# Kernel optimization log

Hardware: AMD Instinct MI355X
Metric: run time of the kernel (lower is better)

Reference implementation:

```python
import jax, jax.numpy as jnp
from jax import lax
import numpy as np

B, N_MEL, T_MEL = 256, 80, 800
R = 16                      # n_frames_per_step
RNN = 1024                  # decoder_rnn_dim
ENC = 256                   # token_embedding_size
MEL_DIM = N_MEL * R         # 1280, == RNN + ENC (LSTMCell input size)
IN_DIM = RNN + ENC          # 1280


def setup_inputs() -> dict:
    key = jax.random.key(0)
    ks = jax.random.split(key, 10)
    s = 0.02
    return {
        "context": jax.random.normal(ks[0], (B, ENC), dtype=jnp.float32),
        "target": jax.random.normal(ks[1], (B, N_MEL, T_MEL), dtype=jnp.float32),
        "W_ih": jax.random.normal(ks[2], (4 * RNN, IN_DIM), dtype=jnp.float32) * s,
        "b_ih": jnp.zeros((4 * RNN,), dtype=jnp.float32),
        "W_hh": jax.random.normal(ks[3], (4 * RNN, RNN), dtype=jnp.float32) * s,
        "b_hh": jnp.zeros((4 * RNN,), dtype=jnp.float32),
        "W_proj": jax.random.normal(ks[4], (MEL_DIM, IN_DIM), dtype=jnp.float32) * s,
        "b_proj": jnp.zeros((MEL_DIM,), dtype=jnp.float32),
        "W_gate": jax.random.normal(ks[5], (1, IN_DIM), dtype=jnp.float32) * s,
        "b_gate": jnp.zeros((1,), dtype=jnp.float32),
    }


def _decoder_forward(context, target, W_ih, b_ih, W_hh, b_hh, W_proj, b_proj, W_gate, b_gate):
    b = context.shape[0]
    n_mel, t_mel = target.shape[1], target.shape[2]
    mel_dim = W_proj.shape[0]
    r = mel_dim // n_mel                      # n_frames_per_step
    T = t_mel // r                            # decoder steps
    rnn = W_hh.shape[1]

    # parse_decoder_inputs: [B, n_mel, T_mel] -> [T, B, mel_dim]
    frames = target.transpose(0, 2, 1).reshape(b, T, mel_dim).transpose(1, 0, 2)
    # step 0 uses the all-zeros go frame; step t>=1 uses target frame t (teacher forcing, p=1)
    inputs = frames.at[0].set(0.0)

    h0 = jnp.zeros((b, rnn), dtype=context.dtype)
    c0 = jnp.zeros((b, rnn), dtype=context.dtype)

    def step(carry, x):
        h, c = carry
        gates = x @ W_ih.T + b_ih + h @ W_hh.T + b_hh   # [B, 4*rnn]
        i, f, g, o = jnp.split(gates, 4, axis=-1)        # torch LSTMCell gate order
        c_new = jax.nn.sigmoid(f) * c + jax.nn.sigmoid(i) * jnp.tanh(g)
        h_new = jax.nn.sigmoid(o) * jnp.tanh(c_new)
        # eval mode: dropout on c is identity
        oc = jnp.concatenate([h_new, context], axis=1)   # [B, rnn+enc]
        mel = oc @ W_proj.T + b_proj                     # [B, mel_dim]
        gate = oc @ W_gate.T + b_gate                    # [B, 1]
        return (h_new, c_new), (mel, gate)

    _, (mels, gates) = lax.scan(step, (h0, c0), inputs)
    # mels: [T, B, mel_dim] -> [B, n_mel, T_mel]
    mel_outputs = mels.transpose(1, 0, 2).reshape(b, T * r, n_mel).transpose(0, 2, 1)
    gate_outputs = gates.transpose(1, 0, 2)              # [B, T, 1]
    return mel_outputs, gate_outputs


def reference(context, target, W_ih, b_ih, W_hh, b_hh, W_proj, b_proj, W_gate, b_gate):
    return _decoder_forward(context, target, W_ih, b_ih, W_hh, b_hh,
                            W_proj, b_proj, W_gate, b_gate)
```

## Files before the change

kernel.cpp:

```cpp
#include <hip/hip_runtime.h>
#include <hip/hip_bf16.h>
#include <math.h>

#define BB     256
#define NMEL   80
#define TMEL   800
#define NFR    16
#define TT     50
#define RNN    1024
#define ENC    256
#define INDIM  1280
#define G4     4096
#define MROWS  (TT*BB)

typedef __attribute__((ext_vector_type(8))) short bf16x8;
typedef __attribute__((ext_vector_type(4))) float f32x4;

#define GAS __attribute__((address_space(1)))
#define LAS __attribute__((address_space(3)))

__device__ __forceinline__ unsigned short f2bf(float f) {
    unsigned int u = __float_as_uint(f);
    u += 0x7FFFu + ((u >> 16) & 1u);
    return (unsigned short)(u >> 16);
}
__device__ __forceinline__ float bf2f(unsigned short s) {
    return __uint_as_float(((unsigned int)s) << 16);
}
__device__ __forceinline__ float fsig(float x) {
    return 1.f / (1.f + __expf(-x));
}
__device__ __forceinline__ float ftanh(float x) {
    return 2.f / (1.f + __expf(-2.f * x)) - 1.f;
}


__global__ void k_f32_to_bf16(const float* __restrict__ src,
                              unsigned short* __restrict__ dst, int n) {
    for (int i = blockIdx.x * blockDim.x + threadIdx.x; i < n;
         i += gridDim.x * blockDim.x)
        dst[i] = f2bf(src[i]);
}

__global__ void k_conv_wph(const float* __restrict__ wproj,
                           unsigned short* __restrict__ dst) {
    const int n = INDIM * RNN;
    for (int i = blockIdx.x * blockDim.x + threadIdx.x; i < n;
         i += gridDim.x * blockDim.x) {
        int mp = i >> 10, k = i & 1023;
        int mel = mp >> 4, fr = mp & 15;
        dst[i] = f2bf(wproj[(fr * NMEL + mel) * INDIM + k]);
    }
}

__global__ void k_frames(const float* __restrict__ target,
                         unsigned short* __restrict__ frames) {
    const int n = TT * BB * INDIM;
    for (int i = blockIdx.x * blockDim.x + threadIdx.x; i < n;
         i += gridDim.x * blockDim.x) {
        int k = i % INDIM;
        int rb = i / INDIM;
        int b = rb & (BB - 1);
        int t = rb >> 8;
        unsigned short v = 0;
        if (t > 0) {
            int mel = k % NMEL, fr = k / NMEL;
            v = f2bf(target[(b * NMEL + mel) * TMEL + t * NFR + fr]);
        }
        frames[i] = v;
    }
}

__global__ void k_ctxproj(const float* __restrict__ context,
                          const float* __restrict__ wproj,
                          const float* __restrict__ bproj,
                          float* __restrict__ ctx) {
    int i = blockIdx.x * blockDim.x + threadIdx.x;
    if (i >= BB * INDIM) return;
    int mp = i % INDIM, b = i / INDIM;
    int mel = mp >> 4, fr = mp & 15;
    int m = fr * NMEL + mel;
    const float* wr = wproj + (size_t)m * INDIM + RNN;
    const float* cb = context + b * ENC;
    float acc = bproj[m];
    for (int e = 0; e < ENC; ++e) acc += cb[e] * wr[e];
    ctx[(size_t)b * INDIM + mp] = acc;
}

__global__ void k_gatectx(const float* __restrict__ context,
                          const float* __restrict__ wgate,
                          const float* __restrict__ bgate,
                          float* __restrict__ gctx) {
    int b = blockIdx.x * blockDim.x + threadIdx.x;
    if (b >= BB) return;
    float acc = bgate[0];
    const float* cb = context + b * ENC;
    for (int e = 0; e < ENC; ++e) acc += cb[e] * wgate[RNN + e];
    gctx[b] = acc;
}

template<int STRIDE, int KDIM>
__device__ __forceinline__ void gemm_core(const unsigned short* __restrict__ A,
                                          const unsigned short* __restrict__ Bw,
                                          int mblk, int nblk,
                                          unsigned short* As, unsigned short* Bs,
                                          f32x4 acc[4][4]) {
    const int tid = threadIdx.x, lane = tid & 63, wid = tid >> 6;
    const int wm = (wid >> 1) * 64, wn = (wid & 1) * 64;
    const int lr = lane & 15, lko = (lane >> 4) * 8;
    const int c0 = wid * 128 + lane;
    const int c1 = c0 + 64;
    const int r0 = c0 >> 2, o0 = (c0 & 3) * 8;
    const int r1 = c1 >> 2, o1 = (c1 & 3) * 8;
    const unsigned short* a0p = A + (size_t)(mblk + r0) * STRIDE + o0;
    const unsigned short* a1p = A + (size_t)(mblk + r1) * STRIDE + o1;
    const unsigned short* b0p = Bw + (size_t)(nblk + r0) * STRIDE + o0;
    const unsigned short* b1p = Bw + (size_t)(nblk + r1) * STRIDE + o1;
    unsigned short* da0 = As + wid * 1024;
    unsigned short* da1 = As + wid * 1024 + 512;
    unsigned short* db0 = Bs + wid * 1024;
    unsigned short* db1 = Bs + wid * 1024 + 512;
    for (int k0 = 0; k0 < KDIM; k0 += 32) {
        __syncthreads();
        __builtin_amdgcn_global_load_lds((const GAS unsigned int*)(a0p + k0),
                                         (LAS unsigned int*)da0, 16, 0, 0);
        __builtin_amdgcn_global_load_lds((const GAS unsigned int*)(a1p + k0),
                                         (LAS unsigned int*)da1, 16, 0, 0);
        __builtin_amdgcn_global_load_lds((const GAS unsigned int*)(b0p + k0),
                                         (LAS unsigned int*)db0, 16, 0, 0);
        __builtin_amdgcn_global_load_lds((const GAS unsigned int*)(b1p + k0),
                                         (LAS unsigned int*)db1, 16, 0, 0);
        __syncthreads();
        bf16x8 af[4], bfv[4];
        #pragma unroll
        for (int mi = 0; mi < 4; ++mi)
            af[mi] = *(const bf16x8*)(As + (wm + mi * 16 + lr) * 32 + lko);
        #pragma unroll
        for (int ni = 0; ni < 4; ++ni)
            bfv[ni] = *(const bf16x8*)(Bs + (wn + ni * 16 + lr) * 32 + lko);
        #pragma unroll
        for (int mi = 0; mi < 4; ++mi)
            #pragma unroll
            for (int ni = 0; ni < 4; ++ni)
                acc[mi][ni] = __builtin_amdgcn_mfma_f32_16x16x32_bf16(
                    af[mi], bfv[ni], acc[mi][ni], 0, 0, 0);
    }
}

__global__ __launch_bounds__(256) void k_gemm_xproj(
    const unsigned short* __restrict__ A,
    const unsigned short* __restrict__ Bw,
    const float* __restrict__ b_ih, const float* __restrict__ b_hh,
    unsigned short* __restrict__ Cout)
{
    __shared__ unsigned short As[4096], Bs[4096];
    f32x4 acc[4][4] = {};
    const int mblk = blockIdx.y * 128, nblk = blockIdx.x * 128;
    gemm_core<INDIM, INDIM>(A, Bw, mblk, nblk, As, Bs, acc);
    const int lane = threadIdx.x & 63, wid = threadIdx.x >> 6;
    const int wm = (wid >> 1) * 64, wn = (wid & 1) * 64, lr = lane & 15;
    #pragma unroll
    for (int ni = 0; ni < 4; ++ni) {
        const int col = nblk + wn + ni * 16 + lr;
        const float bias = b_ih[col] + b_hh[col];
        #pragma unroll
        for (int mi = 0; mi < 4; ++mi) {
            const int row0 = mblk + wm + mi * 16 + (lane >> 4) * 4;
            #pragma unroll
            for (int r = 0; r < 4; ++r)
                Cout[(size_t)(row0 + r) * G4 + col] = f2bf(acc[mi][ni][r] + bias);
        }
    }
}

__global__ __launch_bounds__(256) void k_gemm_mel(
    const unsigned short* __restrict__ A,
    const unsigned short* __restrict__ Bw,
    const float* __restrict__ ctxproj,
    float* __restrict__ out0)
{
    __shared__ unsigned short As[4096], Bs[4096];
    __shared__ float txp[4][16][20];
    f32x4 acc[4][4] = {};
    const int mblk = blockIdx.y * 128, nblk = blockIdx.x * 128;
    gemm_core<RNN, RNN>(A, Bw, mblk, nblk, As, Bs, acc);
    const int lane = threadIdx.x & 63, wid = threadIdx.x >> 6;
    const int wm = (wid >> 1) * 64, wn = (wid & 1) * 64, lr = lane & 15;
    const int rbase = (lane >> 4) * 4;
    const int rowl = lane & 15, fq = lane >> 4;
    #pragma unroll
    for (int mi = 0; mi < 4; ++mi) {
        const int row0 = mblk + wm + mi * 16;
        const int t = row0 >> 8, b0 = row0 & 255;
        #pragma unroll
        for (int ni = 0; ni < 4; ++ni) {
            const int colbase = nblk + wn + ni * 16;
            const int mel = colbase >> 4;
            __syncthreads();
            #pragma unroll
            for (int r = 0; r < 4; ++r)
                txp[wid][rbase + r][lr] = acc[mi][ni][r];
            __syncthreads();
            const int bL = b0 + rowl;
            f32x4 v = *(const f32x4*)&txp[wid][rowl][fq * 4];
            f32x4 cx = *(const f32x4*)(ctxproj + (size_t)bL * INDIM +
                                       mel * 16 + fq * 4);
            *(f32x4*)(out0 + (size_t)(bL * NMEL + mel) * TMEL +
                      t * NFR + fq * 4) = v + cx;
        }
    }
}

__global__ __launch_bounds__(512) void k_step(
    const unsigned short* __restrict__ Whh,
    const unsigned short* __restrict__ xproj_t,
    const unsigned short* __restrict__ h_prev,
    unsigned short* __restrict__ h_next,
    float* __restrict__ c)
{
    __shared__ unsigned short Abuf[3][8192];
    __shared__ unsigned short Bbuf[3][8192];
    __shared__ unsigned short xg[4096];
    __shared__ float cld[64][16];
    __shared__ float gates[4][64][17];
    const int tid = threadIdx.x, lane = tid & 63, w = tid >> 6;
    const int g = w & 3, mh = w >> 2;
    const int n0 = blockIdx.x * 16, m0 = blockIdx.y * 64;
    const int lr = lane & 15, q = lane >> 4;

    const int cc1 = tid, cc2 = tid + 512;
    const int r1 = cc1 >> 4, s1g = (cc1 & 15) ^ (r1 & 15);
    const int r2 = cc2 >> 4, s2g = (cc2 & 15) ^ (r2 & 15);
    const unsigned short* a1src = h_prev + (size_t)(m0 + r1) * RNN + s1g * 8;
    const unsigned short* a2src = h_prev + (size_t)(m0 + r2) * RNN + s2g * 8;
    const unsigned short* b1src = Whh +
        (size_t)((r1 >> 4) * RNN + n0 + (r1 & 15)) * RNN + s1g * 8;
    const unsigned short* b2src = Whh +
        (size_t)((r2 >> 4) * RNN + n0 + (r2 & 15)) * RNN + s2g * 8;
    const unsigned short* xsrc = xproj_t +
        (size_t)(m0 + ((tid >> 1) & 63)) * G4 + (tid >> 7) * RNN + n0 +
        (tid & 1) * 8;
    const float* csrc = c + (size_t)(m0 + (tid >> 2)) * RNN + n0 + (tid & 3) * 4;

#define STAGE(buf, k0) do {                                                    \
    __builtin_amdgcn_global_load_lds((const GAS unsigned int*)(a1src + (k0)),  \
        (LAS unsigned int*)&Abuf[buf][w * 512], 16, 0, 0);                     \
    __builtin_amdgcn_global_load_lds((const GAS unsigned int*)(a2src + (k0)),  \
        (LAS unsigned int*)&Abuf[buf][4096 + w * 512], 16, 0, 0);              \
    __builtin_amdgcn_global_load_lds((const GAS unsigned int*)(b1src + (k0)),  \
        (LAS unsigned int*)&Bbuf[buf][w * 512], 16, 0, 0);                     \
    __builtin_amdgcn_global_load_lds((const GAS unsigned int*)(b2src + (k0)),  \
        (LAS unsigned int*)&Bbuf[buf][4096 + w * 512], 16, 0, 0); } while (0)

    if (w < 4)
        __builtin_amdgcn_global_load_lds((const GAS unsigned int*)csrc,
            (LAS unsigned int*)&cld[w * 16][0], 16, 0, 0);
    __builtin_amdgcn_global_load_lds((const GAS unsigned int*)xsrc,
        (LAS unsigned int*)&xg[w * 512], 16, 0, 0);
    STAGE(0, 0); STAGE(1, 128);

    f32x4 acc[2] = {};
    #pragma unroll
    for (int it = 0; it < 8; ++it) {
        if (it <= 5) STAGE((it + 2) % 3, (it + 2) * 128);
        if (it <= 5)      asm volatile("s_waitcnt vmcnt(8)" ::: "memory");
        else if (it == 6) asm volatile("s_waitcnt vmcnt(4)" ::: "memory");
        else              asm volatile("s_waitcnt vmcnt(0)" ::: "memory");
        asm volatile("s_barrier" ::: "memory");
        __builtin_amdgcn_sched_barrier(0);
        const unsigned short* Ab = Abuf[it % 3];
        const unsigned short* Bb = Bbuf[it % 3];
        #pragma unroll
        for (int ks = 0; ks < 4; ++ks) {
            const int j = ((ks * 4 + q) ^ lr) * 8;
            bf16x8 a0 = *(const bf16x8*)(Ab + (mh * 32 + lr) * 128 + j);
            bf16x8 a1 = *(const bf16x8*)(Ab + (mh * 32 + 16 + lr) * 128 + j);
            bf16x8 bv = *(const bf16x8*)(Bb + (g * 16 + lr) * 128 + j);
            acc[0] = __builtin_amdgcn_mfma_f32_16x16x32_bf16(a0, bv, acc[0], 0, 0, 0);
            acc[1] = __builtin_amdgcn_mfma_f32_16x16x32_bf16(a1, bv, acc[1], 0, 0, 0);
        }
        asm volatile("s_waitcnt lgkmcnt(0)" ::: "memory");
        __builtin_amdgcn_sched_barrier(0);
        asm volatile("s_barrier" ::: "memory");
    }

    #pragma unroll
    for (int mi = 0; mi < 2; ++mi)
        #pragma unroll
        for (int r = 0; r < 4; ++r) {
            const int row = mh * 32 + mi * 16 + q * 4 + r;
            gates[g][row][lr] = acc[mi][r] +
                bf2f(xg[(g * 64 + row) * 16 + lr]);
        }
    __syncthreads();

    #pragma unroll
    for (int q2 = 0; q2 < 2; ++q2) {
        const int e = tid + q2 * 512;
        const int row = e >> 4, col = e & 15;
        const int b = m0 + row, j = n0 + col;
        const float xi = gates[0][row][col];
        const float xf = gates[1][row][col];
        const float xgt = gates[2][row][col];
        const float xo = gates[3][row][col];
        const float si = fsig(xi);
        const float sf = fsig(xf);
        const float so = fsig(xo);
        const float cp = cld[row][col];
        const float cn = sf * cp + si * ftanh(xgt);
        const float hn = so * ftanh(cn);
        c[(size_t)b * RNN + j] = cn;
        h_next[(size_t)b * RNN + j] = f2bf(hn);
    }
#undef STAGE
}

__global__ void k_gate(const unsigned short* __restrict__ h,
                       const float* __restrict__ wgate,
                       const float* __restrict__ gctx,
                       float* __restrict__ out1) {
    const int gw = (blockIdx.x * blockDim.x + threadIdx.x) >> 6;
    const int lane = threadIdx.x & 63;
    if (gw >= MROWS) return;
    const unsigned short* hr = h + (size_t)gw * RNN + lane * 16;
    const float* wr = wgate + lane * 16;
    float acc = 0.f;
    #pragma unroll
    for (int j = 0; j < 16; ++j) acc += bf2f(hr[j]) * wr[j];
    for (int off = 32; off; off >>= 1) acc += __shfl_down(acc, off);
    if (lane == 0) {
        const int t = gw >> 8, b = gw & 255;
        out1[b * TT + t] = acc + gctx[b];
    }
}

static const size_t OFF_WIH   = 0;
static const size_t OFF_WHH   = OFF_WIH   + (size_t)G4 * INDIM * 2;
static const size_t OFF_WPH   = OFF_WHH   + (size_t)G4 * RNN * 2;
static const size_t OFF_FRM   = OFF_WPH   + (size_t)INDIM * RNN * 2;
static const size_t OFF_XPROJ = OFF_FRM   + (size_t)MROWS * INDIM * 2;
static const size_t OFF_HALL  = OFF_XPROJ + (size_t)MROWS * G4 * 2;
static const size_t OFF_C     = OFF_HALL  + (size_t)(TT + 1) * BB * RNN * 2;
static const size_t OFF_CTX   = OFF_C     + (size_t)BB * RNN * 4;
static const size_t OFF_GCTX  = OFF_CTX   + (size_t)BB * INDIM * 4;

extern "C" void kernel_launch(void* const* d_in, const int* in_sizes, int n_in,
                              void* d_out, int out_size, void* d_ws, size_t ws_size,
                              hipStream_t stream) {
    const float* context = (const float*)d_in[0];
    const float* target  = (const float*)d_in[1];
    const float* W_ih    = (const float*)d_in[2];
    const float* b_ih    = (const float*)d_in[3];
    const float* W_hh    = (const float*)d_in[4];
    const float* b_hh    = (const float*)d_in[5];
    const float* W_proj  = (const float*)d_in[6];
    const float* b_proj  = (const float*)d_in[7];
    const float* W_gate  = (const float*)d_in[8];
    const float* b_gate  = (const float*)d_in[9];
    float* out = (float*)d_out;
    char* ws = (char*)d_ws;

    unsigned short* wih_bf  = (unsigned short*)(ws + OFF_WIH);
    unsigned short* whh_bf  = (unsigned short*)(ws + OFF_WHH);
    unsigned short* wph_bf  = (unsigned short*)(ws + OFF_WPH);
    unsigned short* frames  = (unsigned short*)(ws + OFF_FRM);
    unsigned short* xproj   = (unsigned short*)(ws + OFF_XPROJ);
    unsigned short* h_all   = (unsigned short*)(ws + OFF_HALL);
    float*          c_buf   = (float*)(ws + OFF_C);
    float*          ctxproj = (float*)(ws + OFF_CTX);
    float*          gctx    = (float*)(ws + OFF_GCTX);

    hipMemsetAsync(h_all, 0, (size_t)BB * RNN * 2, stream);
    hipMemsetAsync(c_buf, 0, (size_t)BB * RNN * 4, stream);

    k_f32_to_bf16<<<2048, 256, 0, stream>>>(W_ih, wih_bf, G4 * INDIM);
    k_f32_to_bf16<<<2048, 256, 0, stream>>>(W_hh, whh_bf, G4 * RNN);
    k_conv_wph<<<2048, 256, 0, stream>>>(W_proj, wph_bf);
    k_frames<<<2048, 256, 0, stream>>>(target, frames);
    k_ctxproj<<<(BB * INDIM + 255) / 256, 256, 0, stream>>>(context, W_proj,
                                                            b_proj, ctxproj);
    k_gatectx<<<1, 256, 0, stream>>>(context, W_gate, b_gate, gctx);

    k_gemm_xproj<<<dim3(G4 / 128, MROWS / 128), 256, 0, stream>>>(
        frames, wih_bf, b_ih, b_hh, xproj);

    for (int t = 0; t < TT; ++t) {
        k_step<<<dim3(64, 4), 512, 0, stream>>>(
            whh_bf, xproj + (size_t)t * BB * G4,
            h_all + (size_t)t * BB * RNN,
            h_all + (size_t)(t + 1) * BB * RNN, c_buf);
    }

    k_gemm_mel<<<dim3(INDIM / 128, MROWS / 128), 256, 0, stream>>>(
        h_all + (size_t)BB * RNN, wph_bf, ctxproj, out);
    k_gate<<<MROWS / 4, 256, 0, stream>>>(h_all + (size_t)BB * RNN, W_gate,
                                          gctx, out + (size_t)BB * NMEL * TMEL);
}
```

Baseline: 856.9 us.

## Double-buffer and swizzle LDS in bulk GEMMs with 512-thread blocks and K=64 tiles

Replaces the single-buffered K=32 GEMM core used by the input-projection and mel-projection GEMMs with a double-buffered K=64 core. The next tile's global-to-LDS loads are issued before computing on the current one, and the LDS layout is XOR-swizzled to avoid bank conflicts. Blocks grow to 8 waves, each computing a 64x32 sub-tile, so each block has more waves to hide latency. LDS use per block roughly quadruples, and the hand-placed waitcnt and barrier sequencing is fragile.

```diff
diff --git a/kernel.cpp b/kernel.cpp
--- a/kernel.cpp
+++ b/kernel.cpp
@@ -100,72 +100,91 @@
 }
 
 template<int STRIDE, int KDIM>
-__device__ __forceinline__ void gemm_core(const unsigned short* __restrict__ A,
-                                          const unsigned short* __restrict__ Bw,
-                                          int mblk, int nblk,
-                                          unsigned short* As, unsigned short* Bs,
-                                          f32x4 acc[4][4]) {
-    const int tid = threadIdx.x, lane = tid & 63, wid = tid >> 6;
-    const int wm = (wid >> 1) * 64, wn = (wid & 1) * 64;
-    const int lr = lane & 15, lko = (lane >> 4) * 8;
-    const int c0 = wid * 128 + lane;
-    const int c1 = c0 + 64;
-    const int r0 = c0 >> 2, o0 = (c0 & 3) * 8;
-    const int r1 = c1 >> 2, o1 = (c1 & 3) * 8;
-    const unsigned short* a0p = A + (size_t)(mblk + r0) * STRIDE + o0;
-    const unsigned short* a1p = A + (size_t)(mblk + r1) * STRIDE + o1;
-    const unsigned short* b0p = Bw + (size_t)(nblk + r0) * STRIDE + o0;
-    const unsigned short* b1p = Bw + (size_t)(nblk + r1) * STRIDE + o1;
-    unsigned short* da0 = As + wid * 1024;
-    unsigned short* da1 = As + wid * 1024 + 512;
-    unsigned short* db0 = Bs + wid * 1024;
-    unsigned short* db1 = Bs + wid * 1024 + 512;
-    for (int k0 = 0; k0 < KDIM; k0 += 32) {
-        __syncthreads();
-        __builtin_amdgcn_global_load_lds((const GAS unsigned int*)(a0p + k0),
-                                         (LAS unsigned int*)da0, 16, 0, 0);
-        __builtin_amdgcn_global_load_lds((const GAS unsigned int*)(a1p + k0),
-                                         (LAS unsigned int*)da1, 16, 0, 0);
-        __builtin_amdgcn_global_load_lds((const GAS unsigned int*)(b0p + k0),
-                                         (LAS unsigned int*)db0, 16, 0, 0);
-        __builtin_amdgcn_global_load_lds((const GAS unsigned int*)(b1p + k0),
-                                         (LAS unsigned int*)db1, 16, 0, 0);
-        __syncthreads();
-        bf16x8 af[4], bfv[4];
+__device__ __forceinline__ void gemm_core2(const unsigned short* __restrict__ A,
+                                           const unsigned short* __restrict__ Bw,
+                                           int mblk, int nblk,
+                                           unsigned short* As,
+                                           unsigned short* Bs,
+                                           f32x4 acc[4][2]) {
+    const int tid = threadIdx.x, lane = tid & 63, w = tid >> 6;
+    const int lr = lane & 15, q = lane >> 4;
+    const int wm = (w >> 2) * 64, wn = (w & 3) * 32;
+    const int cc1 = tid, cc2 = tid + 512;
+    const int r1 = cc1 >> 3, s1 = ((cc1 & 7) ^ (r1 & 7)) * 8;
+    const int r2 = cc2 >> 3, s2 = ((cc2 & 7) ^ (r2 & 7)) * 8;
+    const unsigned short* a1p = A + (size_t)(mblk + r1) * STRIDE + s1;
+    const unsigned short* a2p = A + (size_t)(mblk + r2) * STRIDE + s2;
+    const unsigned short* b1p = Bw + (size_t)(nblk + r1) * STRIDE + s1;
+    const unsigned short* b2p = Bw + (size_t)(nblk + r2) * STRIDE + s2;
+
+#define GSTAGE(buf, k0) do {                                                   \
+    __builtin_amdgcn_global_load_lds((const GAS unsigned int*)(a1p + (k0)),    \
+        (LAS unsigned int*)(As + (buf) * 8192 + w * 512), 16, 0, 0);           \
+    __builtin_amdgcn_global_load_lds((const GAS unsigned int*)(a2p + (k0)),    \
+        (LAS unsigned int*)(As + (buf) * 8192 + 4096 + w * 512), 16, 0, 0);    \
+    __builtin_amdgcn_global_load_lds((const GAS unsigned int*)(b1p + (k0)),    \
+        (LAS unsigned int*)(Bs + (buf) * 8192 + w * 512), 16, 0, 0);           \
+    __builtin_amdgcn_global_load_lds((const GAS unsigned int*)(b2p + (k0)),    \
+        (LAS unsigned int*)(Bs + (buf) * 8192 + 4096 + w * 512), 16, 0, 0); } while (0)
+
+    constexpr int NIT = KDIM / 64;
+    GSTAGE(0, 0);
+    #pragma unroll 4
+    for (int it = 0; it < NIT; ++it) {
+        if (it < NIT - 1) {
+            GSTAGE((it + 1) & 1, (it + 1) * 64);
+            asm volatile("s_waitcnt vmcnt(4)" ::: "memory");
+        } else {
+            asm volatile("s_waitcnt vmcnt(0)" ::: "memory");
+        }
+        asm volatile("s_barrier" ::: "memory");
+        __builtin_amdgcn_sched_barrier(0);
+        const unsigned short* Ab = As + (it & 1) * 8192;
+        const unsigned short* Bb = Bs + (it & 1) * 8192;
         #pragma unroll
-        for (int mi = 0; mi < 4; ++mi)
-            af[mi] = *(const bf16x8*)(As + (wm + mi * 16 + lr) * 32 + lko);
-        #pragma unroll
-        for (int ni = 0; ni < 4; ++ni)
-            bfv[ni] = *(const bf16x8*)(Bs + (wn + ni * 16 + lr) * 32 + lko);
-        #pragma unroll
-        for (int mi = 0; mi < 4; ++mi)
+        for (int ks = 0; ks < 2; ++ks) {
+            const int j = (((ks * 4 + q) ^ (lr & 7)) * 8);
+            bf16x8 af[4], bv[2];
             #pragma unroll
-            for (int ni = 0; ni < 4; ++ni)
-                acc[mi][ni] = __builtin_amdgcn_mfma_f32_16x16x32_bf16(
-                    af[mi], bfv[ni], acc[mi][ni], 0, 0, 0);
-    }
-}
-
-__global__ __launch_bounds__(256) void k_gemm_xproj(
+            for (int mi = 0; mi < 4; ++mi)
+                af[mi] = *(const bf16x8*)(Ab + (wm + mi * 16 + lr) * 64 + j);
+            #pragma unroll
+            for (int ni = 0; ni < 2; ++ni)
+                bv[ni] = *(const bf16x8*)(Bb + (wn + ni * 16 + lr) * 64 + j);
+            #pragma unroll
+            for (int mi = 0; mi < 4; ++mi)
+                #pragma unroll
+                for (int ni = 0; ni < 2; ++ni)
+                    acc[mi][ni] = __builtin_amdgcn_mfma_f32_16x16x32_bf16(
+                        af[mi], bv[ni], acc[mi][ni], 0, 0, 0);
+        }
+        asm volatile("s_waitcnt lgkmcnt(0)" ::: "memory");
+        __builtin_amdgcn_sched_barrier(0);
+        asm volatile("s_barrier" ::: "memory");
+    }
+#undef GSTAGE
+}
+
+__global__ __launch_bounds__(512) void k_gemm_xproj(
     const unsigned short* __restrict__ A,
     const unsigned short* __restrict__ Bw,
     const float* __restrict__ b_ih, const float* __restrict__ b_hh,
     unsigned short* __restrict__ Cout)
 {
-    __shared__ unsigned short As[4096], Bs[4096];
-    f32x4 acc[4][4] = {};
+    __shared__ unsigned short As[2][8192], Bs[2][8192];
+    f32x4 acc[4][2] = {};
     const int mblk = blockIdx.y * 128, nblk = blockIdx.x * 128;
-    gemm_core<INDIM, INDIM>(A, Bw, mblk, nblk, As, Bs, acc);
-    const int lane = threadIdx.x & 63, wid = threadIdx.x >> 6;
-    const int wm = (wid >> 1) * 64, wn = (wid & 1) * 64, lr = lane & 15;
-    #pragma unroll
-    for (int ni = 0; ni < 4; ++ni) {
+    gemm_core2<INDIM, INDIM>(A, Bw, mblk, nblk, &As[0][0], &Bs[0][0], acc);
+    const int lane = threadIdx.x & 63, w = threadIdx.x >> 6;
+    const int wm = (w >> 2) * 64, wn = (w & 3) * 32;
+    const int lr = lane & 15, q = lane >> 4;
+    #pragma unroll
+    for (int ni = 0; ni < 2; ++ni) {
         const int col = nblk + wn + ni * 16 + lr;
         const float bias = b_ih[col] + b_hh[col];
         #pragma unroll
         for (int mi = 0; mi < 4; ++mi) {
-            const int row0 = mblk + wm + mi * 16 + (lane >> 4) * 4;
+            const int row0 = mblk + wm + mi * 16 + q * 4;
             #pragma unroll
             for (int r = 0; r < 4; ++r)
                 Cout[(size_t)(row0 + r) * G4 + col] = f2bf(acc[mi][ni][r] + bias);
@@ -173,36 +192,37 @@
     }
 }
 
-__global__ __launch_bounds__(256) void k_gemm_mel(
+__global__ __launch_bounds__(512) void k_gemm_mel(
     const unsigned short* __restrict__ A,
     const unsigned short* __restrict__ Bw,
     const float* __restrict__ ctxproj,
     float* __restrict__ out0)
 {
-    __shared__ unsigned short As[4096], Bs[4096];
-    __shared__ float txp[4][16][20];
-    f32x4 acc[4][4] = {};
+    __shared__ unsigned short As[2][8192], Bs[2][8192];
+    __shared__ float txp[8][16][20];
+    f32x4 acc[4][2] = {};
     const int mblk = blockIdx.y * 128, nblk = blockIdx.x * 128;
-    gemm_core<RNN, RNN>(A, Bw, mblk, nblk, As, Bs, acc);
-    const int lane = threadIdx.x & 63, wid = threadIdx.x >> 6;
-    const int wm = (wid >> 1) * 64, wn = (wid & 1) * 64, lr = lane & 15;
-    const int rbase = (lane >> 4) * 4;
+    gemm_core2<RNN, RNN>(A, Bw, mblk, nblk, &As[0][0], &Bs[0][0], acc);
+    const int lane = threadIdx.x & 63, w = threadIdx.x >> 6;
+    const int wm = (w >> 2) * 64, wn = (w & 3) * 32;
+    const int lr = lane & 15, q = lane >> 4;
+    const int rbase = q * 4;
     const int rowl = lane & 15, fq = lane >> 4;
     #pragma unroll
     for (int mi = 0; mi < 4; ++mi) {
         const int row0 = mblk + wm + mi * 16;
         const int t = row0 >> 8, b0 = row0 & 255;
         #pragma unroll
-        for (int ni = 0; ni < 4; ++ni) {
+        for (int ni = 0; ni < 2; ++ni) {
             const int colbase = nblk + wn + ni * 16;
             const int mel = colbase >> 4;
             __syncthreads();
             #pragma unroll
             for (int r = 0; r < 4; ++r)
-                txp[wid][rbase + r][lr] = acc[mi][ni][r];
+                txp[w][rbase + r][lr] = acc[mi][ni][r];
             __syncthreads();
             const int bL = b0 + rowl;
-            f32x4 v = *(const f32x4*)&txp[wid][rowl][fq * 4];
+            f32x4 v = *(const f32x4*)&txp[w][rowl][fq * 4];
             f32x4 cx = *(const f32x4*)(ctxproj + (size_t)bL * INDIM +
                                        mel * 16 + fq * 4);
             *(f32x4*)(out0 + (size_t)(bL * NMEL + mel) * TMEL +
@@ -381,7 +401,7 @@
                                                             b_proj, ctxproj);
     k_gatectx<<<1, 256, 0, stream>>>(context, W_gate, b_gate, gctx);
 
-    k_gemm_xproj<<<dim3(G4 / 128, MROWS / 128), 256, 0, stream>>>(
+    k_gemm_xproj<<<dim3(G4 / 128, MROWS / 128), 512, 0, stream>>>(
         frames, wih_bf, b_ih, b_hh, xproj);
 
     for (int t = 0; t < TT; ++t) {
@@ -391,7 +411,7 @@
             h_all + (size_t)(t + 1) * BB * RNN, c_buf);
     }
 
-    k_gemm_mel<<<dim3(INDIM / 128, MROWS / 128), 256, 0, stream>>>(
+    k_gemm_mel<<<dim3(INDIM / 128, MROWS / 128), 512, 0, stream>>>(
         h_all + (size_t)BB * RNN, wph_bf, ctxproj, out);
     k_gate<<<MROWS / 4, 256, 0, stream>>>(h_all + (size_t)BB * RNN, W_gate,
                                           gctx, out + (size_t)BB * NMEL * TMEL);
```

Result: faster. 825.1 us (-3.7%).
